# Optimization experiments

Hardware: AMD Instinct MI355X
Metric: run time of the kernel (lower is better)

## Reference

```python
import jax, jax.numpy as jnp
import numpy as np

NUM_EMBED = 1024
NUM_HEADS = 16
NUM_LAYER = 8
BLOCK_SIZE = 1024
VOCAB = 32000
B, T = 4, 1024
HEAD_SIZE = NUM_EMBED // NUM_HEADS


def _ln(x, g, b, eps=1e-5):
    mu = jnp.mean(x, axis=-1, keepdims=True)
    var = jnp.var(x, axis=-1, keepdims=True)
    return (x - mu) * jax.lax.rsqrt(var + eps) * g + b


def setup_inputs() -> dict:
    key = jax.random.key(0)
    ks = jax.random.split(key, 16)
    C, L, V = NUM_EMBED, NUM_LAYER, VOCAB
    std = 0.02
    n = lambda k, shp: jax.random.normal(k, shp, jnp.float32) * std
    return {
        "x": jax.random.randint(ks[0], (B, T), 0, V),
        "tok_emb": n(ks[1], (V, C)),
        "pos_emb": n(ks[2], (BLOCK_SIZE, C)),
        "Wq": n(ks[3], (L, C, C)),
        "Wk": n(ks[4], (L, C, C)),
        "Wv": n(ks[5], (L, C, C)),
        "Wproj": n(ks[6], (L, C, C)),
        "bproj": jnp.zeros((L, C), jnp.float32),
        "ln1_g": jnp.ones((L, C), jnp.float32),
        "ln1_b": jnp.zeros((L, C), jnp.float32),
        "ln2_g": jnp.ones((L, C), jnp.float32),
        "ln2_b": jnp.zeros((L, C), jnp.float32),
        "W1": n(ks[7], (L, C, 4 * C)),
        "b1": jnp.zeros((L, 4 * C), jnp.float32),
        "W2": n(ks[8], (L, 4 * C, C)),
        "b2": jnp.zeros((L, C), jnp.float32),
        "lnf_g": jnp.ones((C,), jnp.float32),
        "lnf_b": jnp.zeros((C,), jnp.float32),
        "Whead": n(ks[9], (C, V)),
    }


def _forward(x, tok_emb, pos_emb, Wq, Wk, Wv, Wproj, bproj,
             ln1_g, ln1_b, ln2_g, ln2_b, W1, b1, W2, b2,
             lnf_g, lnf_b, Whead):
    Bc, Tc = x.shape
    H, hs = NUM_HEADS, HEAD_SIZE
    h = tok_emb[x] + pos_emb[:Tc]  # [B,T,C]
    causal = jnp.tril(jnp.ones((Tc, Tc), bool))
    neg_inf = jnp.finfo(h.dtype).min
    for l in range(NUM_LAYER):
        xn = _ln(h, ln1_g[l], ln1_b[l])
        q = (xn @ Wq[l]).reshape(Bc, Tc, H, hs)
        k = (xn @ Wk[l]).reshape(Bc, Tc, H, hs)
        v = (xn @ Wv[l]).reshape(Bc, Tc, H, hs)
        att = jnp.einsum('bqhd,bkhd->bhqk', q, k) * (hs ** -0.5)
        att = jnp.where(causal, att, neg_inf)
        att = jax.nn.softmax(att, axis=-1)  # dropout p=0 in eval
        o = jnp.einsum('bhqk,bkhd->bqhd', att, v).reshape(Bc, Tc, H * hs)
        h = h + o @ Wproj[l] + bproj[l]
        xn = _ln(h, ln2_g[l], ln2_b[l])
        h = h + jax.nn.relu(xn @ W1[l] + b1[l]) @ W2[l] + b2[l]
    h = _ln(h, lnf_g, lnf_b)
    return h @ Whead  # logits [B,T,V]


def reference(x, tok_emb, pos_emb, Wq, Wk, Wv, Wproj, bproj,
              ln1_g, ln1_b, ln2_g, ln2_b, W1, b1, W2, b2,
              lnf_g, lnf_b, Whead):
    return _forward(x, tok_emb, pos_emb, Wq, Wk, Wv, Wproj, bproj,
                    ln1_g, ln1_b, ln2_g, ln2_b, W1, b1, W2, b2,
                    lnf_g, lnf_b, Whead)
```

## Files before the change

kernel.cpp:

```cpp
#include <hip/hip_runtime.h>
#include <stdint.h>
#include <stddef.h>

#define C_DIM 1024
#define T_DIM 1024
#define B_DIM 4
#define L_DIM 8
#define V_DIM 32000
#define HS 64
#define NHEAD 16
#define NROWS (B_DIM * T_DIM)
#define LDQ   3072

typedef __bf16 bf16_t;
typedef __attribute__((ext_vector_type(8))) __bf16 bf16x8;
typedef __attribute__((ext_vector_type(4))) __bf16 bf16x4;
typedef __attribute__((ext_vector_type(4))) float f32x4;
typedef unsigned int u32;
typedef unsigned short u16;

static __device__ __forceinline__ f32x4 mfma16(bf16x8 a, bf16x8 b, f32x4 c) {
    return __builtin_amdgcn_mfma_f32_16x16x32_bf16(a, b, c, 0, 0, 0);
}

static __device__ __forceinline__ void gl_lds16(const bf16_t* g, bf16_t* l) {
    __builtin_amdgcn_global_load_lds(
        (const __attribute__((address_space(1))) u32*)(const void*)g,
        (__attribute__((address_space(3))) u32*)(void*)l, 16, 0, 0);
}

__global__ __launch_bounds__(256) void embed_kernel(
    const int* __restrict__ x, const float* __restrict__ tok,
    const float* __restrict__ pos, float* __restrict__ h) {
    int idx = blockIdx.x * 256 + threadIdx.x;
    int row = idx >> 8;
    int c4  = (idx & 255) * 4;
    int t   = row & (T_DIM - 1);
    int tk  = x[row];
    float4 a = *(const float4*)(tok + (size_t)tk * C_DIM + c4);
    float4 p = *(const float4*)(pos + (size_t)t * C_DIM + c4);
    float4 r;
    r.x = a.x + p.x; r.y = a.y + p.y; r.z = a.z + p.z; r.w = a.w + p.w;
    *(float4*)(h + (size_t)row * C_DIM + c4) = r;
}

static __device__ __forceinline__ void wtr_tile(
    const float* __restrict__ in, bf16_t* __restrict__ out,
    int K, int N, int n0, int k0, int tid) {
    __shared__ float t[64][65];
    int tx = tid & 63, tw = tid >> 6;
#pragma unroll 4
    for (int i = 0; i < 16; ++i) {
        int k = tw * 16 + i;
        t[k][tx] = in[(size_t)(k0 + k) * N + n0 + tx];
    }
    __syncthreads();
#pragma unroll 4
    for (int i = 0; i < 16; ++i) {
        int n = tw * 16 + i;
        out[(size_t)(n0 + n) * K + k0 + tx] = (bf16_t)t[tx][n];
    }
}

__global__ __launch_bounds__(256) void wtr_kernel(
    const float* __restrict__ in, bf16_t* __restrict__ out, int K, int N) {
    wtr_tile(in, out, K, N, blockIdx.x * 64, blockIdx.y * 64, threadIdx.x);
}

__global__ __launch_bounds__(256) void wtr_layer_kernel(
    const float* __restrict__ Wq, const float* __restrict__ Wk,
    const float* __restrict__ Wv, const float* __restrict__ Wp,
    const float* __restrict__ W1, const float* __restrict__ W2,
    bf16_t* __restrict__ qkvT, bf16_t* __restrict__ projT,
    bf16_t* __restrict__ w1T, bf16_t* __restrict__ w2T) {
    int b = blockIdx.x;
    const float* in; bf16_t* out; int K, N, tn, tk;
    if (b < 1024) {
        int which = b >> 8, t = b & 255;
        in  = which == 0 ? Wq : which == 1 ? Wk : which == 2 ? Wv : Wp;
        out = which < 3 ? qkvT + (size_t)which * C_DIM * C_DIM : projT;
        K = C_DIM; N = C_DIM; tn = t & 15; tk = t >> 4;
    } else if (b < 2048) {
        int t = b - 1024; in = W1; out = w1T;
        K = C_DIM; N = 4 * C_DIM; tn = t & 63; tk = t >> 6;
    } else {
        int t = b - 2048; in = W2; out = w2T;
        K = 4 * C_DIM; N = C_DIM; tn = t & 15; tk = t >> 4;
    }
    wtr_tile(in, out, K, N, tn * 64, tk * 64, threadIdx.x);
}

__global__ __launch_bounds__(256) void ln_kernel(
    const float* __restrict__ x, const float* __restrict__ gam,
    const float* __restrict__ bet, bf16_t* __restrict__ out) {
    int wave = threadIdx.x >> 6, lane = threadIdx.x & 63;
    int row  = blockIdx.x * 4 + wave;
    const float* xr = x + (size_t)row * C_DIM;
    float4 v[4];
    float s = 0.f, sq = 0.f;
#pragma unroll
    for (int i = 0; i < 4; ++i) {
        v[i] = *(const float4*)(xr + i * 256 + lane * 4);
        s  += v[i].x + v[i].y + v[i].z + v[i].w;
        sq += v[i].x * v[i].x + v[i].y * v[i].y + v[i].z * v[i].z + v[i].w * v[i].w;
    }
#pragma unroll
    for (int m = 1; m < 64; m <<= 1) {
        s  += __shfl_xor(s, m);
        sq += __shfl_xor(sq, m);
    }
    float mu  = s * (1.f / 1024.f);
    float var = sq * (1.f / 1024.f) - mu * mu;
    float rs  = rsqrtf(var + 1e-5f);
    bf16_t* orow = out + (size_t)row * C_DIM;
#pragma unroll
    for (int i = 0; i < 4; ++i) {
        int c = i * 256 + lane * 4;
        float4 g4 = *(const float4*)(gam + c);
        float4 b4 = *(const float4*)(bet + c);
        bf16x4 o;
        o[0] = (bf16_t)((v[i].x - mu) * rs * g4.x + b4.x);
        o[1] = (bf16_t)((v[i].y - mu) * rs * g4.y + b4.y);
        o[2] = (bf16_t)((v[i].z - mu) * rs * g4.z + b4.z);
        o[3] = (bf16_t)((v[i].w - mu) * rs * g4.w + b4.w);
        *(bf16x4*)(orow + c) = o;
    }
}

template <int MODE>
__global__ __launch_bounds__(256) void gemm_kernel(
    const bf16_t* __restrict__ A, const bf16_t* __restrict__ Bt,
    const float* __restrict__ bias, void* __restrict__ Cout,
    int M, int N, int K) {
    __shared__ bf16_t Asm[2][128 * 32];
    __shared__ bf16_t Bsm[2][128 * 32];

    const int tid  = threadIdx.x;
    const int nwg  = gridDim.x;
    int bid = blockIdx.x;
    if ((nwg & 7) == 0) {
        int cpx = nwg >> 3;
        bid = (bid & 7) * cpx + (bid >> 3);
    }
    const int MT = M >> 7;
    const int mt = bid % MT, nt = bid / MT;
    const int mbase = mt << 7, nbase = nt << 7;
    const int wave = tid >> 6, lane = tid & 63;
    const int lr = lane & 15, lg = lane >> 4;
    const int wm = wave >> 1, wn = wave & 1;
    const int NK = K >> 5;

    const int srow = lane >> 2;
    const int ssw  = (((lane & 3) ^ ((lane >> 3) & 3)) << 3);
    const bf16_t* aRow = A  + (size_t)(mbase + wave * 32 + srow) * K + ssw;
    const bf16_t* bRow = Bt + (size_t)(nbase + wave * 32 + srow) * K + ssw;
    const int ldsW = wave * 1024;

#define STAGE(buf, kt)                                                        \
    do {                                                                      \
        const bf16_t* ag = aRow + (size_t)(kt) * 32;                          \
        const bf16_t* bg = bRow + (size_t)(kt) * 32;                          \
        gl_lds16(ag,            &Asm[buf][ldsW]);                             \
        gl_lds16(ag + 16 * K,   &Asm[buf][ldsW + 512]);                       \
        gl_lds16(bg,            &Bsm[buf][ldsW]);                             \
        gl_lds16(bg + 16 * K,   &Bsm[buf][ldsW + 512]);                       \
    } while (0)

    STAGE(0, 0);
    __syncthreads();

    f32x4 acc[4][4] = {};
    const int rsw = ((lg ^ ((lr >> 1) & 3)) << 3);
    int buf = 0;
    for (int kt = 0; kt < NK; ++kt) {
        if (kt + 1 < NK) STAGE(buf ^ 1, kt + 1);
        bf16x8 af[4], bfr[4];
#pragma unroll
        for (int i = 0; i < 4; ++i)
            af[i] = *(const bf16x8*)&Asm[buf][(wm * 64 + i * 16 + lr) * 32 + rsw];
#pragma unroll
        for (int j = 0; j < 4; ++j)
            bfr[j] = *(const bf16x8*)&Bsm[buf][(wn * 64 + j * 16 + lr) * 32 + rsw];
#pragma unroll
        for (int i = 0; i < 4; ++i)
#pragma unroll
            for (int j = 0; j < 4; ++j)
                acc[i][j] = mfma16(af[i], bfr[j], acc[i][j]);
        __syncthreads();
        buf ^= 1;
    }
#undef STAGE

    float bj[4];
#pragma unroll
    for (int j = 0; j < 4; ++j)
        bj[j] = bias ? bias[nbase + wn * 64 + j * 16 + lr] : 0.0f;
#pragma unroll
    for (int i = 0; i < 4; ++i) {
#pragma unroll
        for (int j = 0; j < 4; ++j) {
            int col = nbase + wn * 64 + j * 16 + lr;
#pragma unroll
            for (int e = 0; e < 4; ++e) {
                int row = mbase + wm * 64 + i * 16 + lg * 4 + e;
                float val = acc[i][j][e] + bj[j];
                size_t off = (size_t)row * N + col;
                if (MODE == 0) {
                    ((bf16_t*)Cout)[off] = (bf16_t)val;
                } else if (MODE == 1) {
                    ((bf16_t*)Cout)[off] = (bf16_t)fmaxf(val, 0.0f);
                } else if (MODE == 2) {
                    ((float*)Cout)[off] += val;
                } else {
                    __builtin_nontemporal_store(val, &((float*)Cout)[off]);
                }
            }
        }
    }
}

template <int MODE>
__global__ __launch_bounds__(512, 4) void gemmW_kernel(
    const bf16_t* __restrict__ A, const bf16_t* __restrict__ Bt,
    const float* __restrict__ bias, void* __restrict__ Cout,
    int M, int N, int K) {
    __shared__ bf16_t As[2][128 * 32];
    __shared__ bf16_t Bs[2][256 * 32];

    const int tid  = threadIdx.x;
    const int nwg  = gridDim.x;
    int bid = blockIdx.x;
    if ((nwg & 7) == 0) {
        int cpx = nwg >> 3;
        bid = (bid & 7) * cpx + (bid >> 3);
    }
    const int MT = M >> 7;
    const int mt = bid % MT, nt = bid / MT;
    const int mbase = mt << 7, nbase = nt << 8;
    const int wave = tid >> 6, lane = tid & 63;
    const int lr = lane & 15, lg = lane >> 4;
    const int wm64 = (wave >> 2) * 64;
    const int wn64 = (wave & 3) * 64;
    const int NK = K >> 5;

    const int srow = tid >> 2;
    const int csrc = (((tid & 3) ^ ((tid >> 3) & 3)) << 3);
    const bf16_t* aPtr = A  + (size_t)(mbase + srow) * K + csrc;
    const bf16_t* b0   = Bt + (size_t)(nbase + srow) * K + csrc;
    const bf16_t* b1   = b0 + (size_t)128 * K;
    const int ldsW = wave * 512;

#define STAGEW(buf, kt)                                                       \
    do {                                                                      \
        gl_lds16(aPtr + (size_t)(kt) * 32, &As[buf][ldsW]);                   \
        gl_lds16(b0   + (size_t)(kt) * 32, &Bs[buf][ldsW]);                   \
        gl_lds16(b1   + (size_t)(kt) * 32, &Bs[buf][4096 + ldsW]);            \
    } while (0)

    STAGEW(0, 0);
    __syncthreads();

    f32x4 acc[4][4] = {};
    const int rofs = ((lg ^ ((lr >> 1) & 3)) << 3);
    int buf = 0;
    for (int kt = 0; kt < NK; ++kt) {
        if (kt + 1 < NK) STAGEW(buf ^ 1, kt + 1);
        bf16x8 af[4], bfr[4];
#pragma unroll
        for (int i = 0; i < 4; ++i)
            af[i] = *(const bf16x8*)&As[buf][(wm64 + i * 16 + lr) * 32 + rofs];
#pragma unroll
        for (int j = 0; j < 4; ++j)
            bfr[j] = *(const bf16x8*)&Bs[buf][(wn64 + j * 16 + lr) * 32 + rofs];
#pragma unroll
        for (int i = 0; i < 4; ++i)
#pragma unroll
            for (int j = 0; j < 4; ++j)
                acc[i][j] = mfma16(af[i], bfr[j], acc[i][j]);
        __syncthreads();
        buf ^= 1;
    }
#undef STAGEW

    float bj[4];
#pragma unroll
    for (int j = 0; j < 4; ++j)
        bj[j] = bias ? bias[nbase + wn64 + j * 16 + lr] : 0.0f;
#pragma unroll
    for (int i = 0; i < 4; ++i) {
#pragma unroll
        for (int j = 0; j < 4; ++j) {
            int col = nbase + wn64 + j * 16 + lr;
#pragma unroll
            for (int e = 0; e < 4; ++e) {
                int row = mbase + wm64 + i * 16 + lg * 4 + e;
                float val = acc[i][j][e] + bj[j];
                size_t off = (size_t)row * N + col;
                if (MODE == 0) {
                    ((bf16_t*)Cout)[off] = (bf16_t)val;
                } else if (MODE == 1) {
                    ((bf16_t*)Cout)[off] = (bf16_t)fmaxf(val, 0.0f);
                } else {
                    __builtin_nontemporal_store(val, &((float*)Cout)[off]);
                }
            }
        }
    }
}

__global__ __launch_bounds__(256) void attn_kernel(
    const bf16_t* __restrict__ Qb, const bf16_t* __restrict__ Kb,
    const bf16_t* __restrict__ Vb, bf16_t* __restrict__ Ob) {
    __shared__ bf16_t Ksm[2][64][72];
    __shared__ bf16_t Vsm[2][64][72];
    __shared__ bf16_t Psm[4][32][72];

    const int tid  = threadIdx.x;
    const int bid  = blockIdx.x;
    const int qt   = 7 - (bid >> 6);
    const int bh   = bid & 63;
    const int hh   = bh & 15;
    const int bb   = bh >> 4;
    const int wave = tid >> 6, lane = tid & 63;
    const int lr = lane & 15, lg = lane >> 4;
    const int qbase = qt * 128 + wave * 32;
    const size_t basei = ((size_t)bb * T_DIM) * LDQ + hh * HS;
    const size_t baseo = ((size_t)bb * T_DIM) * C_DIM + hh * HS;

    bf16x8 qf[2][2];
#pragma unroll
    for (int rb = 0; rb < 2; ++rb) {
        const bf16_t* qrow = Qb + basei + (size_t)(qbase + rb * 16 + lr) * LDQ;
        qf[rb][0] = *(const bf16x8*)(qrow + lg * 8);
        qf[rb][1] = *(const bf16x8*)(qrow + 32 + lg * 8);
    }

    f32x4 o[2][4] = {};
    float m_run[2][4], psum[2][4];
#pragma unroll
    for (int rb = 0; rb < 2; ++rb)
#pragma unroll
        for (int e = 0; e < 4; ++e) { m_run[rb][e] = -1e30f; psum[rb][e] = 0.f; }

    const int krow = tid >> 2, kc = (tid & 3) * 8;
    const bf16_t* kgp = Kb + basei + (size_t)krow * LDQ + kc;
    const int vds = (tid & 7) * 8, vkg = (tid >> 3) * 2;
    const bf16_t* vgp0 = Vb + basei + (size_t)vkg * LDQ + vds;
    const bf16_t* vgp1 = vgp0 + LDQ;

    const int nkt = 2 * qt + 2;

    uint4 k0r, k1r, v0r, v1r;
    k0r = *(const uint4*)(kgp);
    k1r = *(const uint4*)(kgp + 32);
    v0r = *(const uint4*)(vgp0);
    v1r = *(const uint4*)(vgp1);
    *(uint4*)&Ksm[0][krow][kc]      = k0r;
    *(uint4*)&Ksm[0][krow][kc + 32] = k1r;
    {
        const u16* e0 = (const u16*)&v0r;
        const u16* e1 = (const u16*)&v1r;
#pragma unroll
        for (int j = 0; j < 8; ++j)
            *(u32*)&Vsm[0][vds + j][vkg] = (u32)e0[j] | ((u32)e1[j] << 16);
    }
    __syncthreads();

    const float SCL = 0.18033688011112042f;
    for (int kt = 0; kt < nkt; ++kt) {
        const int c = kt & 1;
        if (kt + 1 < nkt) {
            const size_t go = (size_t)(kt + 1) * 64 * LDQ;
            k0r = *(const uint4*)(kgp + go);
            k1r = *(const uint4*)(kgp + go + 32);
            v0r = *(const uint4*)(vgp0 + go);
            v1r = *(const uint4*)(vgp1 + go);
        }

        f32x4 s[2][4];
        __builtin_amdgcn_s_setprio(1);
#pragma unroll
        for (int kk = 0; kk < 4; ++kk) {
            bf16x8 kf0 = *(const bf16x8*)&Ksm[c][kk * 16 + lr][lg * 8];
            bf16x8 kf1 = *(const bf16x8*)&Ksm[c][kk * 16 + lr][32 + lg * 8];
#pragma unroll
            for (int rb = 0; rb < 2; ++rb) {
                f32x4 z = {};
                z = mfma16(qf[rb][0], kf0, z);
                z = mfma16(qf[rb][1], kf1, z);
                s[rb][kk] = z;
            }
        }
        __builtin_amdgcn_s_setprio(0);
        if (kt * 64 + 63 > qbase) {
#pragma unroll
            for (int rb = 0; rb < 2; ++rb)
#pragma unroll
                for (int kk = 0; kk < 4; ++kk)
#pragma unroll
                    for (int e = 0; e < 4; ++e) {
                        int key = kt * 64 + kk * 16 + lr;
                        int qi  = qbase + rb * 16 + lg * 4 + e;
                        float v = s[rb][kk][e] * SCL;
                        s[rb][kk][e] = (key <= qi) ? v : -1e30f;
                    }
        } else {
#pragma unroll
            for (int rb = 0; rb < 2; ++rb)
#pragma unroll
                for (int kk = 0; kk < 4; ++kk)
#pragma unroll
                    for (int e = 0; e < 4; ++e)
                        s[rb][kk][e] *= SCL;
        }

#pragma unroll
        for (int rb = 0; rb < 2; ++rb) {
#pragma unroll
            for (int e = 0; e < 4; ++e) {
                float v = fmaxf(fmaxf(s[rb][0][e], s[rb][1][e]),
                                fmaxf(s[rb][2][e], s[rb][3][e]));
                v = fmaxf(v, __shfl_xor(v, 1));
                v = fmaxf(v, __shfl_xor(v, 2));
                v = fmaxf(v, __shfl_xor(v, 4));
                v = fmaxf(v, __shfl_xor(v, 8));
                float mo = m_run[rb][e];
                if (v > mo + 8.f) {
                    float alpha = exp2f(mo - v);
                    m_run[rb][e] = v;
                    psum[rb][e] *= alpha;
#pragma unroll
                    for (int db = 0; db < 4; ++db)
                        o[rb][db][e] *= alpha;
                }
                float mn = m_run[rb][e];
                float p0 = exp2f(s[rb][0][e] - mn);
                float p1 = exp2f(s[rb][1][e] - mn);
                float p2 = exp2f(s[rb][2][e] - mn);
                float p3 = exp2f(s[rb][3][e] - mn);
                int qrow = rb * 16 + lg * 4 + e;
                Psm[wave][qrow][lr]      = (bf16_t)p0;
                Psm[wave][qrow][16 + lr] = (bf16_t)p1;
                Psm[wave][qrow][32 + lr] = (bf16_t)p2;
                Psm[wave][qrow][48 + lr] = (bf16_t)p3;
                psum[rb][e] += (p0 + p1) + (p2 + p3);
            }
        }

        asm volatile("s_waitcnt lgkmcnt(0)" ::: "memory");
        bf16x8 pf[2][2];
#pragma unroll
        for (int rb = 0; rb < 2; ++rb)
#pragma unroll
            for (int h2 = 0; h2 < 2; ++h2)
                pf[rb][h2] = *(const bf16x8*)&Psm[wave][rb * 16 + lr][h2 * 32 + lg * 8];
        __builtin_amdgcn_s_setprio(1);
#pragma unroll
        for (int h2 = 0; h2 < 2; ++h2)
#pragma unroll
            for (int db = 0; db < 4; ++db) {
                bf16x8 vf = *(const bf16x8*)&Vsm[c][db * 16 + lr][h2 * 32 + lg * 8];
#pragma unroll
                for (int rb = 0; rb < 2; ++rb)
                    o[rb][db] = mfma16(pf[rb][h2], vf, o[rb][db]);
            }
        __builtin_amdgcn_s_setprio(0);

        if (kt + 1 < nkt) {
            const int w = c ^ 1;
            *(uint4*)&Ksm[w][krow][kc]      = k0r;
            *(uint4*)&Ksm[w][krow][kc + 32] = k1r;
            const u16* e0 = (const u16*)&v0r;
            const u16* e1 = (const u16*)&v1r;
#pragma unroll
            for (int j = 0; j < 8; ++j)
                *(u32*)&Vsm[w][vds + j][vkg] = (u32)e0[j] | ((u32)e1[j] << 16);
        }
        __syncthreads();
    }

#pragma unroll
    for (int rb = 0; rb < 2; ++rb)
#pragma unroll
        for (int e = 0; e < 4; ++e) {
            float l = psum[rb][e];
            l += __shfl_xor(l, 1);
            l += __shfl_xor(l, 2);
            l += __shfl_xor(l, 4);
            l += __shfl_xor(l, 8);
            float inv = 1.0f / l;
            bf16_t* orow = Ob + baseo + (size_t)(qbase + rb * 16 + lg * 4 + e) * C_DIM;
#pragma unroll
            for (int db = 0; db < 4; ++db)
                orow[db * 16 + lr] = (bf16_t)(o[rb][db][e] * inv);
        }
}

extern "C" void kernel_launch(void* const* d_in, const int* in_sizes, int n_in,
                              void* d_out, int out_size, void* d_ws, size_t ws_size,
                              hipStream_t stream) {
    const int*   x      = (const int*)d_in[0];
    const float* tok    = (const float*)d_in[1];
    const float* pos    = (const float*)d_in[2];
    const float* Wq     = (const float*)d_in[3];
    const float* Wk     = (const float*)d_in[4];
    const float* Wv     = (const float*)d_in[5];
    const float* Wproj  = (const float*)d_in[6];
    const float* bproj  = (const float*)d_in[7];
    const float* ln1_g  = (const float*)d_in[8];
    const float* ln1_b  = (const float*)d_in[9];
    const float* ln2_g  = (const float*)d_in[10];
    const float* ln2_b  = (const float*)d_in[11];
    const float* W1     = (const float*)d_in[12];
    const float* b1     = (const float*)d_in[13];
    const float* W2     = (const float*)d_in[14];
    const float* b2     = (const float*)d_in[15];
    const float* lnf_g  = (const float*)d_in[16];
    const float* lnf_b  = (const float*)d_in[17];
    const float* Whead  = (const float*)d_in[18];
    float* out = (float*)d_out;

    char* ws = (char*)d_ws;
    float*  h    = (float*)ws;   ws += (size_t)NROWS * C_DIM * 4;
    bf16_t* xn   = (bf16_t*)ws;  ws += (size_t)NROWS * C_DIM * 2;
    bf16_t* qkvb = (bf16_t*)ws;  ws += (size_t)NROWS * LDQ * 2;
    bf16_t* ob   = (bf16_t*)ws;  ws += (size_t)NROWS * C_DIM * 2;
    bf16_t* mid  = (bf16_t*)ws;  ws += (size_t)NROWS * 4 * C_DIM * 2;
    bf16_t* wT   = (bf16_t*)ws;  ws += (size_t)V_DIM * C_DIM * 2;

    const size_t M1 = (size_t)C_DIM * C_DIM;
    bf16_t* qkvT  = wT;
    bf16_t* projT = wT + 3 * M1;
    bf16_t* w1T   = wT + 4 * M1;
    bf16_t* w2T   = wT + 8 * M1;

    dim3 blk(256);
    dim3 blk512(512);

    embed_kernel<<<dim3(NROWS * C_DIM / 1024), blk, 0, stream>>>(x, tok, pos, h);

    for (int l = 0; l < L_DIM; ++l) {
        const size_t wo  = (size_t)l * M1;
        const size_t wo1 = (size_t)l * 4 * M1;

        wtr_layer_kernel<<<dim3(3072), blk, 0, stream>>>(
            Wq + wo, Wk + wo, Wv + wo, Wproj + wo, W1 + wo1, W2 + wo1,
            qkvT, projT, w1T, w2T);

        ln_kernel<<<dim3(NROWS / 4), blk, 0, stream>>>(h, ln1_g + l * C_DIM, ln1_b + l * C_DIM, xn);

        gemmW_kernel<0><<<dim3(32 * 12), blk512, 0, stream>>>(
            xn, qkvT, nullptr, qkvb, NROWS, LDQ, C_DIM);

        attn_kernel<<<dim3(B_DIM * NHEAD * (T_DIM / 128)), blk, 0, stream>>>(
            qkvb, qkvb + C_DIM, qkvb + 2 * C_DIM, ob);

        gemm_kernel<2><<<dim3(32 * 8), blk, 0, stream>>>(ob, projT, bproj + l * C_DIM, h, NROWS, C_DIM, C_DIM);

        ln_kernel<<<dim3(NROWS / 4), blk, 0, stream>>>(h, ln2_g + l * C_DIM, ln2_b + l * C_DIM, xn);

        gemmW_kernel<1><<<dim3(32 * 16), blk512, 0, stream>>>(
            xn, w1T, b1 + (size_t)l * 4 * C_DIM, mid, NROWS, 4 * C_DIM, C_DIM);
        gemm_kernel<2><<<dim3(32 * 8), blk, 0, stream>>>(mid, w2T, b2 + l * C_DIM, h, NROWS, C_DIM, 4 * C_DIM);
    }

    ln_kernel<<<dim3(NROWS / 4), blk, 0, stream>>>(h, lnf_g, lnf_b, xn);
    wtr_kernel<<<dim3(500, 16), blk, 0, stream>>>(Whead, wT, C_DIM, V_DIM);
    gemmW_kernel<3><<<dim3(32 * 125), blk512, 0, stream>>>(
        xn, wT, nullptr, out, NROWS, V_DIM, C_DIM);
}
```

Baseline: 2.648 ms.

## Split attention KV range across two blocks and merge partial softmax results

Each query tile's key range is split into two halves handled by separate blocks (split-K flash attention), doubling the grid from 512 to 1024 blocks. Each block writes an unnormalized fp32 partial output along with its running max and sum, and a new merge kernel combines the two halves with rescaling and writes bf16 output. This targets low occupancy and causal load imbalance on a GPU with many CUs. The cost is extra global traffic for the fp32 partials plus one more kernel launch per layer.

Result: no change. 2.646 ms (-0.1%).

```diff
diff --git a/kernel.cpp b/kernel.cpp
--- a/kernel.cpp
+++ b/kernel.cpp
@@ -11,6 +11,7 @@
 #define NHEAD 16
 #define NROWS (B_DIM * T_DIM)
 #define LDQ   3072
+#define PROWS 65536
 
 typedef __bf16 bf16_t;
 typedef __attribute__((ext_vector_type(8))) __bf16 bf16x8;
@@ -310,22 +311,27 @@
 
 __global__ __launch_bounds__(256) void attn_kernel(
     const bf16_t* __restrict__ Qb, const bf16_t* __restrict__ Kb,
-    const bf16_t* __restrict__ Vb, bf16_t* __restrict__ Ob) {
+    const bf16_t* __restrict__ Vb, float* __restrict__ Opart,
+    float* __restrict__ ML) {
     __shared__ bf16_t Ksm[2][64][72];
     __shared__ bf16_t Vsm[2][64][72];
     __shared__ bf16_t Psm[4][32][72];
 
     const int tid  = threadIdx.x;
     const int bid  = blockIdx.x;
-    const int qt   = 7 - (bid >> 6);
+    const int rank = bid >> 6;
+    const int qt   = 7 - (rank >> 1);
+    const int half = rank & 1;
     const int bh   = bid & 63;
     const int hh   = bh & 15;
     const int bb   = bh >> 4;
+    const int t0   = half ? (qt + 1) : 0;
+    const int t1   = half ? (2 * qt + 2) : (qt + 1);
     const int wave = tid >> 6, lane = tid & 63;
     const int lr = lane & 15, lg = lane >> 4;
     const int qbase = qt * 128 + wave * 32;
     const size_t basei = ((size_t)bb * T_DIM) * LDQ + hh * HS;
-    const size_t baseo = ((size_t)bb * T_DIM) * C_DIM + hh * HS;
+    const int pg = bh * 8 + qt;
 
     bf16x8 qf[2][2];
 #pragma unroll
@@ -348,13 +354,14 @@
     const bf16_t* vgp0 = Vb + basei + (size_t)vkg * LDQ + vds;
     const bf16_t* vgp1 = vgp0 + LDQ;
 
-    const int nkt = 2 * qt + 2;
-
     uint4 k0r, k1r, v0r, v1r;
-    k0r = *(const uint4*)(kgp);
-    k1r = *(const uint4*)(kgp + 32);
-    v0r = *(const uint4*)(vgp0);
-    v1r = *(const uint4*)(vgp1);
+    {
+        const size_t g0 = (size_t)t0 * 64 * LDQ;
+        k0r = *(const uint4*)(kgp + g0);
+        k1r = *(const uint4*)(kgp + g0 + 32);
+        v0r = *(const uint4*)(vgp0 + g0);
+        v1r = *(const uint4*)(vgp1 + g0);
+    }
     *(uint4*)&Ksm[0][krow][kc]      = k0r;
     *(uint4*)&Ksm[0][krow][kc + 32] = k1r;
     {
@@ -367,9 +374,9 @@
     __syncthreads();
 
     const float SCL = 0.18033688011112042f;
-    for (int kt = 0; kt < nkt; ++kt) {
-        const int c = kt & 1;
-        if (kt + 1 < nkt) {
+    for (int kt = t0; kt < t1; ++kt) {
+        const int c = (kt - t0) & 1;
+        if (kt + 1 < t1) {
             const size_t go = (size_t)(kt + 1) * 64 * LDQ;
             k0r = *(const uint4*)(kgp + go);
             k1r = *(const uint4*)(kgp + go + 32);
@@ -466,7 +473,7 @@
             }
         __builtin_amdgcn_s_setprio(0);
 
-        if (kt + 1 < nkt) {
+        if (kt + 1 < t1) {
             const int w = c ^ 1;
             *(uint4*)&Ksm[w][krow][kc]      = k0r;
             *(uint4*)&Ksm[w][krow][kc + 32] = k1r;
@@ -479,6 +486,7 @@
         __syncthreads();
     }
 
+    const size_t prow0 = (size_t)half * PROWS + (size_t)pg * 128 + wave * 32;
 #pragma unroll
     for (int rb = 0; rb < 2; ++rb)
 #pragma unroll
@@ -488,12 +496,36 @@
             l += __shfl_xor(l, 2);
             l += __shfl_xor(l, 4);
             l += __shfl_xor(l, 8);
-            float inv = 1.0f / l;
-            bf16_t* orow = Ob + baseo + (size_t)(qbase + rb * 16 + lg * 4 + e) * C_DIM;
+            size_t row = prow0 + rb * 16 + lg * 4 + e;
+            float* op = Opart + row * 64;
 #pragma unroll
             for (int db = 0; db < 4; ++db)
-                orow[db * 16 + lr] = (bf16_t)(o[rb][db][e] * inv);
-        }
+                op[db * 16 + lr] = o[rb][db][e];
+            if (lr == 0) {
+                ML[row * 2]     = m_run[rb][e];
+                ML[row * 2 + 1] = l;
+            }
+        }
+}
+
+__global__ __launch_bounds__(256) void attn_merge_kernel(
+    const float* __restrict__ Opart, const float* __restrict__ ML,
+    bf16_t* __restrict__ Ob) {
+    int idx = blockIdx.x * 256 + threadIdx.x;
+    int row = idx >> 6, d = idx & 63;
+    float m0 = ML[(size_t)row * 2];
+    float l0 = ML[(size_t)row * 2 + 1];
+    float m1 = ML[((size_t)PROWS + row) * 2];
+    float l1 = ML[((size_t)PROWS + row) * 2 + 1];
+    float M  = fmaxf(m0, m1);
+    float a0 = exp2f(m0 - M), a1 = exp2f(m1 - M);
+    float inv = 1.0f / (a0 * l0 + a1 * l1);
+    float v = (a0 * Opart[(size_t)row * 64 + d] +
+               a1 * Opart[((size_t)PROWS + row) * 64 + d]) * inv;
+    int pg = row >> 7, rloc = row & 127;
+    int bh = pg >> 3, qt = pg & 7;
+    int bb = bh >> 4, hh = bh & 15;
+    Ob[((size_t)bb * T_DIM + qt * 128 + rloc) * C_DIM + hh * HS + d] = (bf16_t)v;
 }
 
 extern "C" void kernel_launch(void* const* d_in, const int* in_sizes, int n_in,
@@ -527,6 +559,8 @@
     bf16_t* ob   = (bf16_t*)ws;  ws += (size_t)NROWS * C_DIM * 2;
     bf16_t* mid  = (bf16_t*)ws;  ws += (size_t)NROWS * 4 * C_DIM * 2;
     bf16_t* wT   = (bf16_t*)ws;  ws += (size_t)V_DIM * C_DIM * 2;
+    float*  opart = (float*)ws;  ws += (size_t)2 * PROWS * 64 * 4;
+    float*  mlbuf = (float*)ws;  ws += (size_t)2 * PROWS * 2 * 4;
 
     const size_t M1 = (size_t)C_DIM * C_DIM;
     bf16_t* qkvT  = wT;
@@ -552,8 +586,10 @@
         gemmW_kernel<0><<<dim3(32 * 12), blk512, 0, stream>>>(
             xn, qkvT, nullptr, qkvb, NROWS, LDQ, C_DIM);
 
-        attn_kernel<<<dim3(B_DIM * NHEAD * (T_DIM / 128)), blk, 0, stream>>>(
-            qkvb, qkvb + C_DIM, qkvb + 2 * C_DIM, ob);
+        attn_kernel<<<dim3(1024), blk, 0, stream>>>(
+            qkvb, qkvb + C_DIM, qkvb + 2 * C_DIM, opart, mlbuf);
+        attn_merge_kernel<<<dim3(2 * PROWS * 64 / 256 / 2), blk, 0, stream>>>(
+            opart, mlbuf, ob);
 
         gemm_kernel<2><<<dim3(32 * 8), blk, 0, stream>>>(ob, projT, bproj + l * C_DIM, h, NROWS, C_DIM, C_DIM);
 
```
